# Optimization experiments

Measured on AMD Instinct MI355X. Metric: run time of the kernel, lower is better.

Reference implementation:

```python
import jax, jax.numpy as jnp
import numpy as np

EPS = 1e-5  # PNA std-aggregator epsilon
N_NODES, N_EDGES, F_DIM, N_LAYERS = 50000, 800000, 64, 3


def setup_inputs() -> dict:
    key = jax.random.key(0)
    ks = jax.random.split(key, 6)
    x = jax.random.normal(ks[0], (N_NODES, F_DIM), jnp.float32)
    edge_index = jax.random.randint(ks[1], (2, N_EDGES), 0, N_NODES, jnp.int32)
    # Per-layer parameters, stacked on a leading layer axis.
    pre_w = jax.random.normal(ks[2], (N_LAYERS, 2 * F_DIM, F_DIM), jnp.float32) / np.sqrt(2 * F_DIM).astype(np.float32)
    pre_b = jnp.zeros((N_LAYERS, F_DIM), jnp.float32)
    post_w = jax.random.normal(ks[3], (N_LAYERS, 13 * F_DIM, F_DIM), jnp.float32) / np.sqrt(13 * F_DIM).astype(np.float32)
    post_b = jnp.zeros((N_LAYERS, F_DIM), jnp.float32)
    lin_w = jax.random.normal(ks[4], (N_LAYERS, F_DIM, F_DIM), jnp.float32) / np.sqrt(F_DIM).astype(np.float32)
    lin_b = jnpp = jnp.zeros((N_LAYERS, F_DIM), jnp.float32)
    return dict(x=x, edge_index=edge_index, pre_w=pre_w, pre_b=pre_b,
                post_w=post_w, post_b=post_b, lin_w=lin_w, lin_b=lin_b)


def reference(x, edge_index, pre_w, pre_b, post_w, post_b, lin_w, lin_b):
    src, dst = edge_index[0], edge_index[1]
    n = x.shape[0]
    # In-degree of aggregation targets (clamped to >=1, as in PyG DegreeScalerAggregation).
    deg = jax.ops.segment_sum(jnp.ones_like(dst, dtype=x.dtype), dst, num_segments=n)
    has_edge = (deg > 0)[:, None]
    deg_c = jnp.maximum(deg, 1.0)[:, None]              # [N,1]
    log_deg = jnp.log(deg_c + 1.0)                      # [N,1]
    avg_log = jnp.mean(log_deg)
    amp = log_deg / avg_log                              # amplification scaler
    att = avg_log / log_deg                              # attenuation scaler

    h = x
    for l in range(pre_w.shape[0]):
        # message: pre_nn(cat([x_i, x_j]))  -> [E, F]
        m = jnp.concatenate([h[dst], h[src]], axis=-1) @ pre_w[l] + pre_b[l]
        # fused multi-aggregator scatter-reduce per target node
        s1 = jax.ops.segment_sum(m, dst, num_segments=n)
        s2 = jax.ops.segment_sum(m * m, dst, num_segments=n)
        mean = s1 / deg_c
        std = jnp.sqrt(jax.nn.relu(s2 / deg_c - mean * mean) + EPS)
        mx = jnp.where(has_edge, jax.ops.segment_max(m, dst, num_segments=n), 0.0)
        mn = jnp.where(has_edge, jax.ops.segment_min(m, dst, num_segments=n), 0.0)
        agg = jnp.concatenate([mean, mx, mn, std], axis=-1)        # [N, 4F]
        scaled = jnp.concatenate([agg, agg * amp, agg * att], -1)  # [N, 12F]
        # post_nn(cat([x, scaled])) then final lin, plus residual shortcut
        out = jnp.concatenate([h, scaled], axis=-1) @ post_w[l] + post_b[l]
        out = out @ lin_w[l] + lin_b[l]
        h = out + h
    return h
```

## Files before the change

### kernel.cpp

```cpp
#include <hip/hip_runtime.h>
#include <math.h>

#define EPSV 1e-5f
#define EPB3 4096
#define NBP 256
#define CAP 6144

typedef short s16x8 __attribute__((ext_vector_type(8)));
typedef float f32x4 __attribute__((ext_vector_type(4)));
typedef unsigned short u16;

#define MFMA(a, b, c) __builtin_amdgcn_mfma_f32_16x16x32_bf16(a, b, c, 0, 0, 0)

__device__ inline u16 f2bf(float f) {
    unsigned u = __float_as_uint(f);
    return (u16)((u + 0x7FFF + ((u >> 16) & 1)) >> 16);
}
__device__ inline float bf2f(u16 h) { return __uint_as_float(((unsigned)h) << 16); }

__device__ inline void split8(const float4& a, const float4& b, s16x8& hv, s16x8& lv) {
    float f[8] = {a.x, a.y, a.z, a.w, b.x, b.y, b.z, b.w};
#pragma unroll
    for (int i = 0; i < 8; ++i) {
        u16 h = f2bf(f[i]);
        hv[i] = (short)h;
        lv[i] = (short)f2bf(f[i] - bf2f(h));
    }
}


__global__ void k_wprep(const float* __restrict__ pre_w, const float* __restrict__ post_w,
                        const float* __restrict__ post_b, const float* __restrict__ lin_w,
                        const float* __restrict__ lin_b, u16* __restrict__ WpT_hi,
                        u16* __restrict__ WpT_lo, u16* __restrict__ WT_hi,
                        u16* __restrict__ WT_lo, float* __restrict__ bpp,
                        int* __restrict__ bucketCur, float* __restrict__ lsum) {
    int l = blockIdx.y, bx = blockIdx.x, t = threadIdx.x;
    if (bx < 320) {
        int k = bx, j = t;
        int third = j >> 6, c = j & 63;
        float out = 0.f;
        int r = -1;
        if (k < 64) r = (third == 0) ? k : -1;
        else        r = 64 + third * 256 + (k - 64);
        if (r >= 0) {
            const float* pw = post_w + (size_t)(l * 832 + r) * 64;
            const float* lw = lin_w + (size_t)l * 64 * 64;
            float s = 0.f;
            for (int kk = 0; kk < 64; ++kk) s += pw[kk] * lw[kk * 64 + c];
            out = s;
        }
        u16 h = f2bf(out);
        size_t o = ((size_t)l * 192 + j) * 320 + k;
        WT_hi[o] = h;
        WT_lo[o] = f2bf(out - bf2f(h));
    } else if (bx < 448) {
        if (t < 64) {
            int c = bx - 320, k = t;
            float v = pre_w[(size_t)l * 8192 + (size_t)(k + (c >= 64 ? 64 : 0)) * 64 + (c & 63)];
            u16 h = f2bf(v);
            size_t o = ((size_t)l * 128 + c) * 64 + k;
            WpT_hi[o] = h;
            WpT_lo[o] = f2bf(v - bf2f(h));
        }
    } else if (bx == 448) {
        if (t < 64) {
            int c = t;
            const float* pb = post_b + l * 64;
            const float* lw = lin_w + (size_t)l * 64 * 64;
            float s = lin_b[l * 64 + c];
            for (int k = 0; k < 64; ++k) s += pb[k] * lw[k * 64 + c];
            bpp[l * 64 + c] = s;
        }
    } else if (l == 0) {
        int i = (bx - 449) * 192 + t;
        if (i < NBP) bucketCur[i] = 0;
        if (i == 0) *lsum = 0.f;
    }
}

__global__ __launch_bounds__(512) void k_bucket3(const int* __restrict__ src,
                                                 const int* __restrict__ dst, int E,
                                                 int* __restrict__ bucketCursor,
                                                 unsigned* __restrict__ edgeTmp) {
    __shared__ int cnt[NBP], loff[NBP], lpos[NBP], gbase[NBP], sbuf[NBP];
    __shared__ unsigned stage[EPB3];
    int t = threadIdx.x;
    int base = blockIdx.x * EPB3;
    int cntE = min(EPB3, E - base);
    if (t < NBP) cnt[t] = 0;
    __syncthreads();
    unsigned ed[8];
#pragma unroll
    for (int j = 0; j < 8; ++j) {
        int idx = j * 512 + t;
        if (idx < cntE) {
            int e = base + idx;
            unsigned s = (unsigned)src[e];
            unsigned d = (unsigned)dst[e];
            ed[j] = ((d >> 8) << 24) | ((d & 255u) << 16) | s;
            atomicAdd(&cnt[d >> 8], 1);
        } else ed[j] = 0xFFFFFFFFu;
    }
    __syncthreads();
    if (t < NBP) sbuf[t] = cnt[t];
    __syncthreads();
    for (int o = 1; o < NBP; o <<= 1) {
        int v = 0;
        if (t < NBP && t >= o) v = sbuf[t - o];
        __syncthreads();
        if (t < NBP) sbuf[t] += v;
        __syncthreads();
    }
    if (t < NBP) {
        loff[t] = sbuf[t] - cnt[t];
        lpos[t] = sbuf[t] - cnt[t];
        gbase[t] = (cnt[t] > 0) ? atomicAdd(&bucketCursor[t], cnt[t]) : 0;
    }
    __syncthreads();
#pragma unroll
    for (int j = 0; j < 8; ++j) {
        if (ed[j] != 0xFFFFFFFFu) {
            int b = ed[j] >> 24;
            int p = atomicAdd(&lpos[b], 1);
            stage[p] = ed[j];
        }
    }
    __syncthreads();
    for (int i = t; i < cntE; i += 512) {
        unsigned pr = stage[i];
        int b = pr >> 24;
        int pos = gbase[b] + (i - loff[b]);
        if (pos < CAP) edgeTmp[(size_t)b * CAP + pos] = pr;
    }
}

__global__ __launch_bounds__(512) void k_csort2(const unsigned* __restrict__ edgeTmp,
                                                const int* __restrict__ bucketCur,
                                                int* __restrict__ deg,
                                                int* __restrict__ offs,
                                                float* __restrict__ lsum,
                                                u16* __restrict__ srcSorted,
                                                int N, int E, int NB) {
    __shared__ int bcnt[NBP], sbuf[NBP], lcur[NBP], lofs[NBP];
    __shared__ float fred[256];
    __shared__ u16 stageSrc[CAP];
    __shared__ int e0s;
    int b = blockIdx.x, t = threadIdx.x;
    int n0 = b << 8;
    int nodes = min(256, N - n0);
    if (t < NBP) bcnt[t] = (t < NB) ? bucketCur[t] : 0;
    if (t < NBP) lcur[t] = 0;
    __syncthreads();
    if (t < NBP) sbuf[t] = bcnt[t];
    __syncthreads();
    for (int o = 1; o < NBP; o <<= 1) {
        int v = 0;
        if (t < NBP && t >= o) v = sbuf[t - o];
        __syncthreads();
        if (t < NBP) sbuf[t] += v;
        __syncthreads();
    }
    if (t == 0) e0s = sbuf[b] - bcnt[b];
    __syncthreads();
    int e0 = e0s;
    int cnt = min(bcnt[b], CAP);
    const unsigned* ebase = edgeTmp + (size_t)b * CAP;
    for (int i = t; i < cnt; i += 512) atomicAdd(&lcur[(ebase[i] >> 16) & 255], 1);
    __syncthreads();
    float ls = 0.f;
    if (t < 256) {
        if (t < nodes) {
            int d = lcur[t];
            deg[n0 + t] = d;
            ls = logf(fmaxf((float)d, 1.f) + 1.f);
        }
        fred[t] = ls;
    }
    if (t < NBP) sbuf[t] = lcur[t];
    __syncthreads();
    for (int o = 1; o < NBP; o <<= 1) {
        int v = 0;
        if (t < NBP && t >= o) v = sbuf[t - o];
        __syncthreads();
        if (t < NBP) sbuf[t] += v;
        __syncthreads();
    }
    if (t < NBP) lofs[t] = sbuf[t] - lcur[t];
    if (t < nodes) offs[n0 + t] = e0 + (sbuf[t] - lcur[t]);
    if (b == 0 && t == 0) offs[N] = E;
    __syncthreads();
    for (int o = 128; o > 0; o >>= 1) {
        if (t < o) fred[t] += fred[t + o];
        __syncthreads();
    }
    if (t == 0) atomicAdd(lsum, fred[0]);
    if (t < NBP) sbuf[t] = 0;
    __syncthreads();
    for (int i = t; i < cnt; i += 512) {
        unsigned p = ebase[i];
        int dl = (p >> 16) & 255;
        int r = atomicAdd(&sbuf[dl], 1);
        stageSrc[lofs[dl] + r] = (u16)(p & 0xFFFFu);
    }
    __syncthreads();
    for (int i = t; i < cnt; i += 512) srcSorted[e0 + i] = stageSrc[i];
}


__global__ __launch_bounds__(256) void k_gemm1(const float* __restrict__ h,
                                               const u16* __restrict__ WpT_hi,
                                               const u16* __restrict__ WpT_lo,
                                               const float* __restrict__ pre_b,
                                               u16* __restrict__ Ph, u16* __restrict__ Qh,
                                               int M) {
    __shared__ u16 Ah[64 * 72], Al[64 * 72];
    __shared__ u16 Bh[128 * 72], Bl[128 * 72];
    int t = threadIdx.x, wid = t >> 6, lane = t & 63;
    int rows0 = blockIdx.x * 64;
    int quad = lane >> 4, l16 = lane & 15;
    int wm = wid & 1, wn = wid >> 1;

#pragma unroll
    for (int it = 0; it < 2; ++it) {
        int task = it * 256 + t;
        int r = task >> 3, seg = task & 7;
        int row = rows0 + r;
        float4 v0 = make_float4(0.f, 0.f, 0.f, 0.f), v1 = v0;
        if (row < M) {
            v0 = *(const float4*)&h[(size_t)row * 64 + seg * 8];
            v1 = *(const float4*)&h[(size_t)row * 64 + seg * 8 + 4];
        }
        s16x8 hv, lv;
        split8(v0, v1, hv, lv);
        *(s16x8*)&Ah[r * 72 + seg * 8] = hv;
        *(s16x8*)&Al[r * 72 + seg * 8] = lv;
    }
#pragma unroll
    for (int it = 0; it < 4; ++it) {
        int task = it * 256 + t;
        int c = task >> 3, seg = task & 7;
        *(s16x8*)&Bh[c * 72 + seg * 8] = *(const s16x8*)&WpT_hi[(size_t)c * 64 + seg * 8];
        *(s16x8*)&Bl[c * 72 + seg * 8] = *(const s16x8*)&WpT_lo[(size_t)c * 64 + seg * 8];
    }
    __syncthreads();

    f32x4 acc[2][4];
#pragma unroll
    for (int mt = 0; mt < 2; ++mt)
#pragma unroll
        for (int tt = 0; tt < 4; ++tt) acc[mt][tt] = (f32x4){0.f, 0.f, 0.f, 0.f};

#pragma unroll
    for (int c = 0; c < 2; ++c) {
        s16x8 ah[2], al[2];
#pragma unroll
        for (int mt = 0; mt < 2; ++mt) {
            int r = wm * 32 + mt * 16 + l16;
            ah[mt] = *(s16x8*)&Ah[r * 72 + c * 32 + quad * 8];
            al[mt] = *(s16x8*)&Al[r * 72 + c * 32 + quad * 8];
        }
#pragma unroll
        for (int tt = 0; tt < 4; ++tt) {
            int cc = wn * 64 + tt * 16 + l16;
            s16x8 bh = *(s16x8*)&Bh[cc * 72 + c * 32 + quad * 8];
            s16x8 bl = *(s16x8*)&Bl[cc * 72 + c * 32 + quad * 8];
#pragma unroll
            for (int mt = 0; mt < 2; ++mt) {
                acc[mt][tt] = MFMA(ah[mt], bh, acc[mt][tt]);
                acc[mt][tt] = MFMA(ah[mt], bl, acc[mt][tt]);
                if (wn == 0) acc[mt][tt] = MFMA(al[mt], bh, acc[mt][tt]);
            }
        }
    }

#pragma unroll
    for (int mt = 0; mt < 2; ++mt)
#pragma unroll
        for (int tt = 0; tt < 4; ++tt) {
            int col = wn * 64 + tt * 16 + l16;
#pragma unroll
            for (int r = 0; r < 4; ++r) {
                int row = rows0 + wm * 32 + mt * 16 + quad * 4 + r;
                if (row >= M) continue;
                float v = acc[mt][tt][r];
                if (col < 64) Ph[(size_t)row * 64 + col] = f2bf(v + pre_b[col]);
                else          Qh[(size_t)row * 64 + (col - 64)] = f2bf(v);
            }
        }
}

__global__ __launch_bounds__(256) void k_agg(const u16* __restrict__ Ph,
                                             const u16* __restrict__ Qh,
                                             const int* __restrict__ offs,
                                             const u16* __restrict__ ss,
                                             u16* __restrict__ AGGh, int N) {
    int w = threadIdx.x >> 6, lane = threadIdx.x & 63;
    int i0 = blockIdx.x * 8 + w * 2;
    int i1 = i0 + 1;
    if (i0 >= N) return;
    int beg0 = offs[i0], end0 = offs[i0 + 1];
    int beg1 = 0, end1 = 0;
    if (i1 < N) { beg1 = offs[i1]; end1 = offs[i1 + 1]; }
    float sum0 = 0.f, sqa0 = 0.f, sqb0 = 0.f, mx0 = -3.4e38f, mn0 = 3.4e38f;
    float sum1 = 0.f, sqa1 = 0.f, sqb1 = 0.f, mx1 = -3.4e38f, mn1 = 3.4e38f;
    int e0 = beg0, e1 = beg1;
    while (e0 + 8 <= end0 && e1 + 8 <= end1) {
        float qa[8], qb[8];
#pragma unroll
        for (int j = 0; j < 8; ++j) qa[j] = bf2f(Qh[((int)ss[e0 + j] << 6) + lane]);
#pragma unroll
        for (int j = 0; j < 8; ++j) qb[j] = bf2f(Qh[((int)ss[e1 + j] << 6) + lane]);
        sum0 += ((qa[0] + qa[1]) + (qa[2] + qa[3])) + ((qa[4] + qa[5]) + (qa[6] + qa[7]));
        sqa0 = fmaf(qa[0], qa[0], fmaf(qa[2], qa[2], fmaf(qa[4], qa[4], fmaf(qa[6], qa[6], sqa0))));
        sqb0 = fmaf(qa[1], qa[1], fmaf(qa[3], qa[3], fmaf(qa[5], qa[5], fmaf(qa[7], qa[7], sqb0))));
        mx0 = fmaxf(mx0, fmaxf(fmaxf(fmaxf(qa[0], qa[1]), fmaxf(qa[2], qa[3])),
                               fmaxf(fmaxf(qa[4], qa[5]), fmaxf(qa[6], qa[7]))));
        mn0 = fminf(mn0, fminf(fminf(fminf(qa[0], qa[1]), fminf(qa[2], qa[3])),
                               fminf(fminf(qa[4], qa[5]), fminf(qa[6], qa[7]))));
        sum1 += ((qb[0] + qb[1]) + (qb[2] + qb[3])) + ((qb[4] + qb[5]) + (qb[6] + qb[7]));
        sqa1 = fmaf(qb[0], qb[0], fmaf(qb[2], qb[2], fmaf(qb[4], qb[4], fmaf(qb[6], qb[6], sqa1))));
        sqb1 = fmaf(qb[1], qb[1], fmaf(qb[3], qb[3], fmaf(qb[5], qb[5], fmaf(qb[7], qb[7], sqb1))));
        mx1 = fmaxf(mx1, fmaxf(fmaxf(fmaxf(qb[0], qb[1]), fmaxf(qb[2], qb[3])),
                               fmaxf(fmaxf(qb[4], qb[5]), fmaxf(qb[6], qb[7]))));
        mn1 = fminf(mn1, fminf(fminf(fminf(qb[0], qb[1]), fminf(qb[2], qb[3])),
                               fminf(fminf(qb[4], qb[5]), fminf(qb[6], qb[7]))));
        e0 += 8; e1 += 8;
    }
    for (; e0 + 4 <= end0; e0 += 4) {
        float q0 = bf2f(Qh[((int)ss[e0 + 0] << 6) + lane]);
        float q1 = bf2f(Qh[((int)ss[e0 + 1] << 6) + lane]);
        float q2 = bf2f(Qh[((int)ss[e0 + 2] << 6) + lane]);
        float q3 = bf2f(Qh[((int)ss[e0 + 3] << 6) + lane]);
        sum0 += (q0 + q1) + (q2 + q3);
        sqa0 = fmaf(q0, q0, fmaf(q2, q2, sqa0));
        sqb0 = fmaf(q1, q1, fmaf(q3, q3, sqb0));
        mx0 = fmaxf(mx0, fmaxf(fmaxf(q0, q1), fmaxf(q2, q3)));
        mn0 = fminf(mn0, fminf(fminf(q0, q1), fminf(q2, q3)));
    }
    for (; e1 + 4 <= end1; e1 += 4) {
        float q0 = bf2f(Qh[((int)ss[e1 + 0] << 6) + lane]);
        float q1 = bf2f(Qh[((int)ss[e1 + 1] << 6) + lane]);
        float q2 = bf2f(Qh[((int)ss[e1 + 2] << 6) + lane]);
        float q3 = bf2f(Qh[((int)ss[e1 + 3] << 6) + lane]);
        sum1 += (q0 + q1) + (q2 + q3);
        sqa1 = fmaf(q0, q0, fmaf(q2, q2, sqa1));
        sqb1 = fmaf(q1, q1, fmaf(q3, q3, sqb1));
        mx1 = fmaxf(mx1, fmaxf(fmaxf(q0, q1), fmaxf(q2, q3)));
        mn1 = fminf(mn1, fminf(fminf(q0, q1), fminf(q2, q3)));
    }
    for (; e0 < end0; ++e0) {
        float q = bf2f(Qh[((int)ss[e0] << 6) + lane]);
        sum0 += q; sqa0 = fmaf(q, q, sqa0);
        mx0 = fmaxf(mx0, q); mn0 = fminf(mn0, q);
    }
    for (; e1 < end1; ++e1) {
        float q = bf2f(Qh[((int)ss[e1] << 6) + lane]);
        sum1 += q; sqa1 = fmaf(q, q, sqa1);
        mx1 = fmaxf(mx1, q); mn1 = fminf(mn1, q);
    }
    {
        int deg = end0 - beg0;
        float sq = sqa0 + sqb0;
        float p = bf2f(Ph[(i0 << 6) + lane]);
        float dc = fmaxf((float)deg, 1.f);
        float eq = sum0 / dc;
        float var = fmaxf(sq / dc - eq * eq, 0.f);
        float sd = sqrtf(var + EPSV);
        float mean, vmx, vmn;
        if (deg > 0) { mean = p + eq; vmx = p + mx0; vmn = p + mn0; }
        else         { mean = 0.f; vmx = 0.f; vmn = 0.f; }
        int o = (i0 << 8) + lane;
        AGGh[o] = f2bf(mean);
        AGGh[o + 64] = f2bf(vmx);
        AGGh[o + 128] = f2bf(vmn);
        AGGh[o + 192] = f2bf(sd);
    }
    if (i1 < N) {
        int deg = end1 - beg1;
        float sq = sqa1 + sqb1;
        float p = bf2f(Ph[(i1 << 6) + lane]);
        float dc = fmaxf((float)deg, 1.f);
        float eq = sum1 / dc;
        float var = fmaxf(sq / dc - eq * eq, 0.f);
        float sd = sqrtf(var + EPSV);
        float mean, vmx, vmn;
        if (deg > 0) { mean = p + eq; vmx = p + mx1; vmn = p + mn1; }
        else         { mean = 0.f; vmx = 0.f; vmn = 0.f; }
        int o = (i1 << 8) + lane;
        AGGh[o] = f2bf(mean);
        AGGh[o + 64] = f2bf(vmx);
        AGGh[o + 128] = f2bf(vmn);
        AGGh[o + 192] = f2bf(sd);
    }
}

__global__ __launch_bounds__(512) void k_gemm2(const float* __restrict__ hIn,
                                               const u16* __restrict__ AGGh,
                                               const u16* __restrict__ WT_hi,
                                               const u16* __restrict__ WT_lo,
                                               const float* __restrict__ bpp,
                                               const int* __restrict__ degp,
                                               const float* __restrict__ lsum,
                                               float* __restrict__ hOut,
                                               int doNext,
                                               const u16* __restrict__ WpN_hi,
                                               const u16* __restrict__ WpN_lo,
                                               const float* __restrict__ pre_bN,
                                               u16* __restrict__ PhN,
                                               u16* __restrict__ QhN, int M) {
    __shared__ u16 Ah[128 * 40], Al[128 * 40];
    __shared__ u16 Bh[192 * 40], Bl[192 * 40];
    int t = threadIdx.x, wid = t >> 6, lane = t & 63;
    int rows0 = blockIdx.x * 128;
    int quad = lane >> 4, l16 = lane & 15;
    int wm = wid & 3, wn = wid >> 2;

    f32x4 acc[2][6];
#pragma unroll
    for (int mt = 0; mt < 2; ++mt)
#pragma unroll
        for (int tt = 0; tt < 6; ++tt) acc[mt][tt] = (f32x4){0.f, 0.f, 0.f, 0.f};

#pragma unroll
    for (int chunk = 0; chunk < 2; ++chunk) {
        {
            int r = t >> 2, seg = t & 3;
            int row = rows0 + r;
            float4 v0 = make_float4(0.f, 0.f, 0.f, 0.f), v1 = v0;
            if (row < M) {
                v0 = *(const float4*)&hIn[(size_t)row * 64 + chunk * 32 + seg * 8];
                v1 = *(const float4*)&hIn[(size_t)row * 64 + chunk * 32 + seg * 8 + 4];
            }
            s16x8 hv, lv;
            split8(v0, v1, hv, lv);
            *(s16x8*)&Ah[r * 40 + seg * 8] = hv;
            *(s16x8*)&Al[r * 40 + seg * 8] = lv;
        }
        if (t < 256) {
            int c = t >> 2, seg = t & 3;
            int k0g = chunk * 32;
            *(s16x8*)&Bh[c * 40 + seg * 8] = *(const s16x8*)&WT_hi[(size_t)c * 320 + k0g + seg * 8];
            *(s16x8*)&Bl[c * 40 + seg * 8] = *(const s16x8*)&WT_lo[(size_t)c * 320 + k0g + seg * 8];
        }
        __syncthreads();

        s16x8 ah[2], al[2];
#pragma unroll
        for (int mt = 0; mt < 2; ++mt) {
            int r = wm * 32 + mt * 16 + l16;
            ah[mt] = *(s16x8*)&Ah[r * 40 + quad * 8];
            al[mt] = *(s16x8*)&Al[r * 40 + quad * 8];
        }
#pragma unroll
        for (int cg = 0; cg < 2; ++cg) {
            int cc = wn * 32 + cg * 16 + l16;
            s16x8 bh = *(s16x8*)&Bh[cc * 40 + quad * 8];
            s16x8 bl = *(s16x8*)&Bl[cc * 40 + quad * 8];
#pragma unroll
            for (int mt = 0; mt < 2; ++mt) {
                acc[mt][cg] = MFMA(ah[mt], bh, acc[mt][cg]);
                acc[mt][cg] = MFMA(al[mt], bh, acc[mt][cg]);
                acc[mt][cg] = MFMA(ah[mt], bl, acc[mt][cg]);
            }
        }
        __syncthreads();
    }

    for (int chunk = 0; chunk < 8; ++chunk) {
        {
            int r = t >> 2, seg = t & 3;
            int row = rows0 + r;
            s16x8 v = (s16x8){0, 0, 0, 0, 0, 0, 0, 0};
            if (row < M) v = *(const s16x8*)&AGGh[(size_t)row * 256 + chunk * 32 + seg * 8];
            *(s16x8*)&Ah[r * 40 + seg * 8] = v;
        }
        {
            int k0g = 64 + chunk * 32;
#pragma unroll
            for (int it = 0; it < 2; ++it) {
                int task = it * 512 + t;
                if (task < 768) {
                    int c = task >> 2, seg = task & 3;
                    *(s16x8*)&Bh[c * 40 + seg * 8] = *(const s16x8*)&WT_hi[(size_t)c * 320 + k0g + seg * 8];
                    *(s16x8*)&Bl[c * 40 + seg * 8] = *(const s16x8*)&WT_lo[(size_t)c * 320 + k0g + seg * 8];
                }
            }
        }
        __syncthreads();

        s16x8 ah[2];
#pragma unroll
        for (int mt = 0; mt < 2; ++mt) {
            int r = wm * 32 + mt * 16 + l16;
            ah[mt] = *(s16x8*)&Ah[r * 40 + quad * 8];
        }
#pragma unroll
        for (int tt = 0; tt < 6; ++tt) {
            int cc = wn * 32 + (tt & 1) * 16 + (tt >> 1) * 64 + l16;
            s16x8 bh = *(s16x8*)&Bh[cc * 40 + quad * 8];
            s16x8 bl = *(s16x8*)&Bl[cc * 40 + quad * 8];
#pragma unroll
            for (int mt = 0; mt < 2; ++mt) {
                acc[mt][tt] = MFMA(ah[mt], bh, acc[mt][tt]);
                acc[mt][tt] = MFMA(ah[mt], bl, acc[mt][tt]);
            }
        }
        __syncthreads();
    }

    float hv[2][2][4];
    float avg = *lsum / (float)M;
#pragma unroll
    for (int mt = 0; mt < 2; ++mt)
#pragma unroll
        for (int r = 0; r < 4; ++r) {
            int row = rows0 + wm * 32 + mt * 16 + quad * 4 + r;
            float am = 1.f, at = 1.f, hin0 = 0.f, hin1 = 0.f;
            if (row < M) {
                float dc = fmaxf((float)degp[row], 1.f);
                float ld = logf(dc + 1.f);
                am = ld / avg;
                at = avg / ld;
                hin0 = hIn[(size_t)row * 64 + wn * 32 + l16];
                hin1 = hIn[(size_t)row * 64 + wn * 32 + 16 + l16];
            }
#pragma unroll
            for (int cg = 0; cg < 2; ++cg) {
                int col = wn * 32 + cg * 16 + l16;
                float v = acc[mt][cg][r] + am * acc[mt][cg + 2][r] + at * acc[mt][cg + 4][r]
                        + (cg == 0 ? hin0 : hin1) + bpp[col];
                hv[mt][cg][r] = v;
                if (row < M) hOut[(size_t)row * 64 + col] = v;
            }
        }

    if (doNext) {
        f32x4 acc2[2][4];
#pragma unroll
        for (int mt = 0; mt < 2; ++mt)
#pragma unroll
            for (int tt = 0; tt < 4; ++tt) acc2[mt][tt] = (f32x4){0.f, 0.f, 0.f, 0.f};

#pragma unroll
        for (int chunk = 0; chunk < 2; ++chunk) {
            {
                int c = t >> 2, seg = t & 3;
                *(s16x8*)&Bh[c * 40 + seg * 8] = *(const s16x8*)&WpN_hi[(size_t)c * 64 + chunk * 32 + seg * 8];
                *(s16x8*)&Bl[c * 40 + seg * 8] = *(const s16x8*)&WpN_lo[(size_t)c * 64 + chunk * 32 + seg * 8];
            }
            if (wn == chunk) {
#pragma unroll
                for (int mt = 0; mt < 2; ++mt)
#pragma unroll
                    for (int cg = 0; cg < 2; ++cg) {
                        int lc = cg * 16 + l16;
#pragma unroll
                        for (int r = 0; r < 4; ++r) {
                            int rl = wm * 32 + mt * 16 + quad * 4 + r;
                            float v = hv[mt][cg][r];
                            u16 hi = f2bf(v);
                            Ah[rl * 40 + lc] = hi;
                            Al[rl * 40 + lc] = f2bf(v - bf2f(hi));
                        }
                    }
            }
            __syncthreads();

            s16x8 ah[2], al[2];
#pragma unroll
            for (int mt = 0; mt < 2; ++mt) {
                int r = wm * 32 + mt * 16 + l16;
                ah[mt] = *(s16x8*)&Ah[r * 40 + quad * 8];
                al[mt] = *(s16x8*)&Al[r * 40 + quad * 8];
            }
#pragma unroll
            for (int tt = 0; tt < 4; ++tt) {
                int cc = wn * 64 + tt * 16 + l16;
                s16x8 bh = *(s16x8*)&Bh[cc * 40 + quad * 8];
                s16x8 bl = *(s16x8*)&Bl[cc * 40 + quad * 8];
#pragma unroll
                for (int mt = 0; mt < 2; ++mt) {
                    acc2[mt][tt] = MFMA(ah[mt], bh, acc2[mt][tt]);
                    acc2[mt][tt] = MFMA(ah[mt], bl, acc2[mt][tt]);
                    if (wn == 0) acc2[mt][tt] = MFMA(al[mt], bh, acc2[mt][tt]);
                }
            }
            __syncthreads();
        }

#pragma unroll
        for (int mt = 0; mt < 2; ++mt)
#pragma unroll
            for (int tt = 0; tt < 4; ++tt) {
                int col = wn * 64 + tt * 16 + l16;
#pragma unroll
                for (int r = 0; r < 4; ++r) {
                    int row = rows0 + wm * 32 + mt * 16 + quad * 4 + r;
                    if (row >= M) continue;
                    float v = acc2[mt][tt][r];
                    if (col < 64) PhN[(size_t)row * 64 + col] = f2bf(v + pre_bN[col]);
                    else          QhN[(size_t)row * 64 + (col - 64)] = f2bf(v);
                }
            }
    }
}


extern "C" void kernel_launch(void* const* d_in, const int* in_sizes, int n_in,
                              void* d_out, int out_size, void* d_ws, size_t ws_size,
                              hipStream_t stream) {
    const float* x      = (const float*)d_in[0];
    const int*   ei     = (const int*)d_in[1];
    const float* pre_w  = (const float*)d_in[2];
    const float* pre_b  = (const float*)d_in[3];
    const float* post_w = (const float*)d_in[4];
    const float* post_b = (const float*)d_in[5];
    const float* lin_w  = (const float*)d_in[6];
    const float* lin_b  = (const float*)d_in[7];

    const int N = in_sizes[0] / 64;
    const int E = in_sizes[1] / 2;
    const int L = in_sizes[2] / (128 * 64);

    const int* srcIdx = ei;
    const int* dstIdx = ei + E;

    char* ws = (char*)d_ws;
    size_t off = 0;
    auto alloc = [&](size_t bytes) {
        void* p = ws + off;
        off += (bytes + 255) & ~(size_t)255;
        return p;
    };
    int*      deg        = (int*)alloc((size_t)N * 4);
    int*      offs       = (int*)alloc((size_t)(N + 1) * 4);
    u16*      srcSorted  = (u16*)alloc((size_t)E * 2);
    unsigned* edgeTmp    = (unsigned*)alloc((size_t)NBP * CAP * 4);
    int*      bucketCur  = (int*)alloc(NBP * 4);
    float*    lsum       = (float*)alloc(256);
    u16*      WpT_hi     = (u16*)alloc((size_t)L * 128 * 64 * 2);
    u16*      WpT_lo     = (u16*)alloc((size_t)L * 128 * 64 * 2);
    u16*      WT_hi      = (u16*)alloc((size_t)L * 192 * 320 * 2);
    u16*      WT_lo      = (u16*)alloc((size_t)L * 192 * 320 * 2);
    float*    bpp        = (float*)alloc((size_t)L * 64 * 4);
    u16*      Ph         = (u16*)alloc((size_t)N * 64 * 2);
    u16*      Qh         = (u16*)alloc((size_t)N * 64 * 2);
    u16*      AGGh       = (u16*)alloc((size_t)N * 256 * 2);
    float*    hA         = (float*)alloc((size_t)N * 64 * 4);
    float*    hB         = (float*)alloc((size_t)N * 64 * 4);
    (void)ws_size;

    int NB = (N + 255) >> 8;
    int NB1 = (E + EPB3 - 1) / EPB3;
    int initBlk = (NBP + 191) / 192;

    k_wprep<<<dim3(449 + initBlk, L), 192, 0, stream>>>(
        pre_w, post_w, post_b, lin_w, lin_b, WpT_hi, WpT_lo, WT_hi, WT_lo, bpp,
        bucketCur, lsum);
    k_bucket3<<<NB1, 512, 0, stream>>>(srcIdx, dstIdx, E, bucketCur, edgeTmp);
    k_csort2<<<NB, 512, 0, stream>>>(edgeTmp, bucketCur, deg, offs, lsum,
                                     srcSorted, N, E, NB);

    int gblk = (N + 63) / 64;
    int gblk2 = (N + 127) / 128;
    k_gemm1<<<gblk, 256, 0, stream>>>(x, WpT_hi, WpT_lo, pre_b, Ph, Qh, N);

    const float* hIn = x;
    float* hbuf[2] = {hA, hB};
    for (int l = 0; l < L; ++l) {
        float* hOut = (l == L - 1) ? (float*)d_out : hbuf[l & 1];
        int dn = (l < L - 1) ? 1 : 0;
        int ln = dn ? (l + 1) : 0;
        k_agg<<<(N + 7) / 8, 256, 0, stream>>>(Ph, Qh, offs, srcSorted, AGGh, N);
        k_gemm2<<<gblk2, 512, 0, stream>>>(hIn, AGGh,
                                           WT_hi + (size_t)l * 192 * 320,
                                           WT_lo + (size_t)l * 192 * 320,
                                           bpp + (size_t)l * 64,
                                           deg, lsum, hOut, dn,
                                           WpT_hi + (size_t)ln * 128 * 64,
                                           WpT_lo + (size_t)ln * 128 * 64,
                                           pre_b + (size_t)ln * 64,
                                           Ph, Qh, N);
        hIn = hOut;
    }
}
```

Baseline: 305.8 us.

## Restructure aggregation: one node per wave, 4 edge groups with vectorized gathers

```diff
diff --git a/kernel.cpp b/kernel.cpp
--- a/kernel.cpp
+++ b/kernel.cpp
@@ -2,13 +2,14 @@
 #include <math.h>
 
 #define EPSV 1e-5f
-#define EPB3 4096
+#define EPB3 2048
 #define NBP 256
 #define CAP 6144
 
 typedef short s16x8 __attribute__((ext_vector_type(8)));
 typedef float f32x4 __attribute__((ext_vector_type(4)));
 typedef unsigned short u16;
+typedef unsigned short u16x4 __attribute__((ext_vector_type(4)));
 
 #define MFMA(a, b, c) __builtin_amdgcn_mfma_f32_16x16x32_bf16(a, b, c, 0, 0, 0)
 
@@ -90,9 +91,9 @@
     int cntE = min(EPB3, E - base);
     if (t < NBP) cnt[t] = 0;
     __syncthreads();
-    unsigned ed[8];
-#pragma unroll
-    for (int j = 0; j < 8; ++j) {
+    unsigned ed[4];
+#pragma unroll
+    for (int j = 0; j < 4; ++j) {
         int idx = j * 512 + t;
         if (idx < cntE) {
             int e = base + idx;
@@ -119,7 +120,7 @@
     }
     __syncthreads();
 #pragma unroll
-    for (int j = 0; j < 8; ++j) {
+    for (int j = 0; j < 4; ++j) {
         if (ed[j] != 0xFFFFFFFFu) {
             int b = ed[j] >> 24;
             int p = atomicAdd(&lpos[b], 1);
@@ -296,103 +297,92 @@
                                              const u16* __restrict__ ss,
                                              u16* __restrict__ AGGh, int N) {
     int w = threadIdx.x >> 6, lane = threadIdx.x & 63;
-    int i0 = blockIdx.x * 8 + w * 2;
-    int i1 = i0 + 1;
-    if (i0 >= N) return;
-    int beg0 = offs[i0], end0 = offs[i0 + 1];
-    int beg1 = 0, end1 = 0;
-    if (i1 < N) { beg1 = offs[i1]; end1 = offs[i1 + 1]; }
-    float sum0 = 0.f, sqa0 = 0.f, sqb0 = 0.f, mx0 = -3.4e38f, mn0 = 3.4e38f;
-    float sum1 = 0.f, sqa1 = 0.f, sqb1 = 0.f, mx1 = -3.4e38f, mn1 = 3.4e38f;
-    int e0 = beg0, e1 = beg1;
-    while (e0 + 8 <= end0 && e1 + 8 <= end1) {
-        float qa[8], qb[8];
-#pragma unroll
-        for (int j = 0; j < 8; ++j) qa[j] = bf2f(Qh[((int)ss[e0 + j] << 6) + lane]);
-#pragma unroll
-        for (int j = 0; j < 8; ++j) qb[j] = bf2f(Qh[((int)ss[e1 + j] << 6) + lane]);
-        sum0 += ((qa[0] + qa[1]) + (qa[2] + qa[3])) + ((qa[4] + qa[5]) + (qa[6] + qa[7]));
-        sqa0 = fmaf(qa[0], qa[0], fmaf(qa[2], qa[2], fmaf(qa[4], qa[4], fmaf(qa[6], qa[6], sqa0))));
-        sqb0 = fmaf(qa[1], qa[1], fmaf(qa[3], qa[3], fmaf(qa[5], qa[5], fmaf(qa[7], qa[7], sqb0))));
-        mx0 = fmaxf(mx0, fmaxf(fmaxf(fmaxf(qa[0], qa[1]), fmaxf(qa[2], qa[3])),
-                               fmaxf(fmaxf(qa[4], qa[5]), fmaxf(qa[6], qa[7]))));
-        mn0 = fminf(mn0, fminf(fminf(fminf(qa[0], qa[1]), fminf(qa[2], qa[3])),
-                               fminf(fminf(qa[4], qa[5]), fminf(qa[6], qa[7]))));
-        sum1 += ((qb[0] + qb[1]) + (qb[2] + qb[3])) + ((qb[4] + qb[5]) + (qb[6] + qb[7]));
-        sqa1 = fmaf(qb[0], qb[0], fmaf(qb[2], qb[2], fmaf(qb[4], qb[4], fmaf(qb[6], qb[6], sqa1))));
-        sqb1 = fmaf(qb[1], qb[1], fmaf(qb[3], qb[3], fmaf(qb[5], qb[5], fmaf(qb[7], qb[7], sqb1))));
-        mx1 = fmaxf(mx1, fmaxf(fmaxf(fmaxf(qb[0], qb[1]), fmaxf(qb[2], qb[3])),
-                               fmaxf(fmaxf(qb[4], qb[5]), fmaxf(qb[6], qb[7]))));
-        mn1 = fminf(mn1, fminf(fminf(fminf(qb[0], qb[1]), fminf(qb[2], qb[3])),
-                               fminf(fminf(qb[4], qb[5]), fminf(qb[6], qb[7]))));
-        e0 += 8; e1 += 8;
-    }
-    for (; e0 + 4 <= end0; e0 += 4) {
-        float q0 = bf2f(Qh[((int)ss[e0 + 0] << 6) + lane]);
-        float q1 = bf2f(Qh[((int)ss[e0 + 1] << 6) + lane]);
-        float q2 = bf2f(Qh[((int)ss[e0 + 2] << 6) + lane]);
-        float q3 = bf2f(Qh[((int)ss[e0 + 3] << 6) + lane]);
-        sum0 += (q0 + q1) + (q2 + q3);
-        sqa0 = fmaf(q0, q0, fmaf(q2, q2, sqa0));
-        sqb0 = fmaf(q1, q1, fmaf(q3, q3, sqb0));
-        mx0 = fmaxf(mx0, fmaxf(fmaxf(q0, q1), fmaxf(q2, q3)));
-        mn0 = fminf(mn0, fminf(fminf(q0, q1), fminf(q2, q3)));
-    }
-    for (; e1 + 4 <= end1; e1 += 4) {
-        float q0 = bf2f(Qh[((int)ss[e1 + 0] << 6) + lane]);
-        float q1 = bf2f(Qh[((int)ss[e1 + 1] << 6) + lane]);
-        float q2 = bf2f(Qh[((int)ss[e1 + 2] << 6) + lane]);
-        float q3 = bf2f(Qh[((int)ss[e1 + 3] << 6) + lane]);
-        sum1 += (q0 + q1) + (q2 + q3);
-        sqa1 = fmaf(q0, q0, fmaf(q2, q2, sqa1));
-        sqb1 = fmaf(q1, q1, fmaf(q3, q3, sqb1));
-        mx1 = fmaxf(mx1, fmaxf(fmaxf(q0, q1), fmaxf(q2, q3)));
-        mn1 = fminf(mn1, fminf(fminf(q0, q1), fminf(q2, q3)));
-    }
-    for (; e0 < end0; ++e0) {
-        float q = bf2f(Qh[((int)ss[e0] << 6) + lane]);
-        sum0 += q; sqa0 = fmaf(q, q, sqa0);
-        mx0 = fmaxf(mx0, q); mn0 = fminf(mn0, q);
-    }
-    for (; e1 < end1; ++e1) {
-        float q = bf2f(Qh[((int)ss[e1] << 6) + lane]);
-        sum1 += q; sqa1 = fmaf(q, q, sqa1);
-        mx1 = fmaxf(mx1, q); mn1 = fminf(mn1, q);
-    }
-    {
-        int deg = end0 - beg0;
-        float sq = sqa0 + sqb0;
-        float p = bf2f(Ph[(i0 << 6) + lane]);
-        float dc = fmaxf((float)deg, 1.f);
-        float eq = sum0 / dc;
-        float var = fmaxf(sq / dc - eq * eq, 0.f);
-        float sd = sqrtf(var + EPSV);
-        float mean, vmx, vmn;
-        if (deg > 0) { mean = p + eq; vmx = p + mx0; vmn = p + mn0; }
-        else         { mean = 0.f; vmx = 0.f; vmn = 0.f; }
-        int o = (i0 << 8) + lane;
-        AGGh[o] = f2bf(mean);
-        AGGh[o + 64] = f2bf(vmx);
-        AGGh[o + 128] = f2bf(vmn);
-        AGGh[o + 192] = f2bf(sd);
-    }
-    if (i1 < N) {
-        int deg = end1 - beg1;
-        float sq = sqa1 + sqb1;
-        float p = bf2f(Ph[(i1 << 6) + lane]);
-        float dc = fmaxf((float)deg, 1.f);
-        float eq = sum1 / dc;
-        float var = fmaxf(sq / dc - eq * eq, 0.f);
-        float sd = sqrtf(var + EPSV);
-        float mean, vmx, vmn;
-        if (deg > 0) { mean = p + eq; vmx = p + mx1; vmn = p + mn1; }
-        else         { mean = 0.f; vmx = 0.f; vmn = 0.f; }
-        int o = (i1 << 8) + lane;
-        AGGh[o] = f2bf(mean);
-        AGGh[o + 64] = f2bf(vmx);
-        AGGh[o + 128] = f2bf(vmn);
-        AGGh[o + 192] = f2bf(sd);
-    }
+    int node = blockIdx.x * 4 + w;
+    if (node >= N) return;
+    int beg = offs[node], end = offs[node + 1];
+    int g = lane >> 4;
+    int f4 = (lane & 15) << 2;
+
+    float sum0 = 0.f, sum1 = 0.f, sum2 = 0.f, sum3 = 0.f;
+    float sq0 = 0.f, sq1 = 0.f, sq2 = 0.f, sq3 = 0.f;
+    float mx0 = -3.4e38f, mx1 = -3.4e38f, mx2 = -3.4e38f, mx3 = -3.4e38f;
+    float mn0 = 3.4e38f, mn1 = 3.4e38f, mn2 = 3.4e38f, mn3 = 3.4e38f;
+
+    const u16* qb = Qh + f4;
+
+#define ACC4(LO, HI)                                                        \
+    {                                                                       \
+        float q0 = __uint_as_float((LO) << 16);                             \
+        float q1 = __uint_as_float((LO) & 0xFFFF0000u);                     \
+        float q2 = __uint_as_float((HI) << 16);                             \
+        float q3 = __uint_as_float((HI) & 0xFFFF0000u);                     \
+        sum0 += q0; sq0 = fmaf(q0, q0, sq0);                                \
+        mx0 = fmaxf(mx0, q0); mn0 = fminf(mn0, q0);                         \
+        sum1 += q1; sq1 = fmaf(q1, q1, sq1);                                \
+        mx1 = fmaxf(mx1, q1); mn1 = fminf(mn1, q1);                         \
+        sum2 += q2; sq2 = fmaf(q2, q2, sq2);                                \
+        mx2 = fmaxf(mx2, q2); mn2 = fminf(mn2, q2);                         \
+        sum3 += q3; sq3 = fmaf(q3, q3, sq3);                                \
+        mx3 = fmaxf(mx3, q3); mn3 = fminf(mn3, q3);                         \
+    }
+
+    int e = beg + g;
+    int nfull = (end - beg) >> 3;
+    for (int it = 0; it < nfull; ++it, e += 8) {
+        int s0 = ss[e];
+        int s1 = ss[e + 4];
+        uint2 a = *(const uint2*)(qb + ((size_t)s0 << 6));
+        uint2 b = *(const uint2*)(qb + ((size_t)s1 << 6));
+        ACC4(a.x, a.y);
+        ACC4(b.x, b.y);
+    }
+    int rem = (end - beg) - (nfull << 3);
+    if (g < rem) {
+        int s0 = ss[e];
+        uint2 a = *(const uint2*)(qb + ((size_t)s0 << 6));
+        ACC4(a.x, a.y);
+    }
+    if (g + 4 < rem) {
+        int s1 = ss[e + 4];
+        uint2 b = *(const uint2*)(qb + ((size_t)s1 << 6));
+        ACC4(b.x, b.y);
+    }
+#undef ACC4
+
+#define CMBA(v) v += __shfl_xor(v, 16); v += __shfl_xor(v, 32);
+#define CMBX(v) v = fmaxf(v, __shfl_xor(v, 16)); v = fmaxf(v, __shfl_xor(v, 32));
+#define CMBN(v) v = fminf(v, __shfl_xor(v, 16)); v = fminf(v, __shfl_xor(v, 32));
+    CMBA(sum0) CMBA(sum1) CMBA(sum2) CMBA(sum3)
+    CMBA(sq0) CMBA(sq1) CMBA(sq2) CMBA(sq3)
+    CMBX(mx0) CMBX(mx1) CMBX(mx2) CMBX(mx3)
+    CMBN(mn0) CMBN(mn1) CMBN(mn2) CMBN(mn3)
+#undef CMBA
+#undef CMBX
+#undef CMBN
+
+    int deg = end - beg;
+    float dc = fmaxf((float)deg, 1.f);
+    u16 o0, o1, o2, o3;
+    if (g == 3) {
+        float e0 = sum0 / dc, e1 = sum1 / dc, e2 = sum2 / dc, e3 = sum3 / dc;
+        o0 = f2bf(sqrtf(fmaxf(sq0 / dc - e0 * e0, 0.f) + EPSV));
+        o1 = f2bf(sqrtf(fmaxf(sq1 / dc - e1 * e1, 0.f) + EPSV));
+        o2 = f2bf(sqrtf(fmaxf(sq2 / dc - e2 * e2, 0.f) + EPSV));
+        o3 = f2bf(sqrtf(fmaxf(sq3 / dc - e3 * e3, 0.f) + EPSV));
+    } else if (deg > 0) {
+        const u16* prow = Ph + ((size_t)node << 6) + f4;
+        u16x4 pv = *(const u16x4*)prow;
+        float p0 = bf2f(pv.x), p1 = bf2f(pv.y), p2 = bf2f(pv.z), p3 = bf2f(pv.w);
+        float a0, a1, a2, a3;
+        if (g == 0)      { a0 = sum0 / dc; a1 = sum1 / dc; a2 = sum2 / dc; a3 = sum3 / dc; }
+        else if (g == 1) { a0 = mx0; a1 = mx1; a2 = mx2; a3 = mx3; }
+        else             { a0 = mn0; a1 = mn1; a2 = mn2; a3 = mn3; }
+        o0 = f2bf(p0 + a0); o1 = f2bf(p1 + a1); o2 = f2bf(p2 + a2); o3 = f2bf(p3 + a3);
+    } else {
+        o0 = o1 = o2 = o3 = 0;
+    }
+    u16x4 ov = {o0, o1, o2, o3};
+    *(u16x4*)&AGGh[((size_t)node << 8) + (g << 6) + f4] = ov;
 }
 
 __global__ __launch_bounds__(512) void k_gemm2(const float* __restrict__ hIn,
@@ -672,7 +662,7 @@
         float* hOut = (l == L - 1) ? (float*)d_out : hbuf[l & 1];
         int dn = (l < L - 1) ? 1 : 0;
         int ln = dn ? (l + 1) : 0;
-        k_agg<<<(N + 7) / 8, 256, 0, stream>>>(Ph, Qh, offs, srcSorted, AGGh, N);
+        k_agg<<<(N + 3) / 4, 256, 0, stream>>>(Ph, Qh, offs, srcSorted, AGGh, N);
         k_gemm2<<<gblk2, 512, 0, stream>>>(hIn, AGGh,
                                            WT_hi + (size_t)l * 192 * 320,
                                            WT_lo + (size_t)l * 192 * 320,
```

Result: slower. 329.3 us (+7.7%).
